# Kernel tuning notes

Hardware: AMD Instinct MI355X
Metric: run time of the kernel (lower is better)

## Reference

```python
import jax, jax.numpy as jnp
import numpy as np

K = 4                 # max_block_size (depthwise conv kernel size)
BLOCKS = (1, 2, 3, 4) # block sizes, offset 0
DS = 4                # downsample_factor
BLOCK_MULT = 12       # lcm(1,2,3,4)
DIM = 512
NUM_TOKENS = 256


def setup_inputs() -> dict:
    key = jax.random.key(0)
    ks = jax.random.split(key, 8)
    b, n = 4, 4096
    s = 0.02
    return {
        "x": jax.random.randint(ks[0], (b, n), 0, NUM_TOKENS),
        "emb": jax.random.normal(ks[1], (NUM_TOKENS, DIM), dtype=jnp.float32) * s,
        "conv_w": jax.random.normal(ks[2], (DIM, K), dtype=jnp.float32) * s,   # depthwise Conv1d weight [d,1,K] squeezed
        "conv_b": jax.random.normal(ks[3], (DIM,), dtype=jnp.float32) * s,
        "proj_w": jax.random.normal(ks[4], (DIM, DIM), dtype=jnp.float32) * s,  # 1x1 conv == linear [out,in]
        "proj_b": jax.random.normal(ks[5], (DIM,), dtype=jnp.float32) * s,
        "score_w": jax.random.normal(ks[6], (DIM,), dtype=jnp.float32) * s,     # nn.Linear(dim,1)
        "score_b": jax.random.normal(ks[7], (), dtype=jnp.float32) * s,
    }


def reference(x, emb, conv_w, conv_b, proj_w, proj_b, score_w, score_b):
    b, n = x.shape
    h = emb[x]  # [b, n, d] token embedding (gather)

    # pos_conv: pad (K-1) at sequence end, depthwise conv (valid), then pointwise proj
    hp = jnp.pad(h, ((0, 0), (0, K - 1), (0, 0)))
    y = conv_b + sum(hp[:, k:k + n, :] * conv_w[:, k] for k in range(K))  # [b, n, d]
    h = y @ proj_w.T + proj_b

    # pad sequence to multiple of lcm of block sizes
    L = -(-n // BLOCK_MULT) * BLOCK_MULT
    h = jnp.pad(h, ((0, 0), (0, L - n), (0, 0)))

    # multi-scale block mean pooling, upsampled back to length L
    reprs = []
    for bs in BLOCKS:
        r = h.reshape(b, L // bs, bs, DIM).mean(axis=2)     # [b, L/bs, d]
        reprs.append(jnp.repeat(r, bs, axis=1))             # [b, L, d]
    block_reprs = jnp.stack(reprs, axis=2)                  # [b, L, nb, d]

    # per-position block scores
    scores = block_reprs @ score_w + score_b                # [b, L, nb]
    scores = jax.nn.softmax(scores, axis=2)

    # consensus attention over positions (d = nb = len(BLOCKS))
    sim = jnp.einsum('bid,bjd->bij', scores, scores)        # [b, L, L]
    attn = jax.nn.softmax(sim, axis=-1)
    scores = jnp.einsum('bij,bjm->bim', attn, scores)       # [b, L, nb]

    # fuse block representations and downsample
    out = jnp.einsum('bnkd,bnk->bnd', block_reprs, scores)  # [b, L, d]
    m = -(-n // DS) * DS                                    # == n (4096 divisible by 4)
    out = out[:, :m].reshape(b, m // DS, DS, DIM).mean(axis=2)
    return out
```

## Files before the change

### kernel.cpp

```cpp
#include <hip/hip_runtime.h>
#include <hip/hip_bf16.h>

#define B_ 4
#define N_ 4096
#define L_ 4104
#define D_ 512
#define CH2 129
#define BK 64
#define NF 210

typedef __attribute__((ext_vector_type(8))) short bf16x8;
typedef __attribute__((ext_vector_type(4))) float f32x4;

__device__ __forceinline__ float bf2f(unsigned short u) {
  union { unsigned u; float f; } c; c.u = ((unsigned)u) << 16; return c.f;
}

__global__ __launch_bounds__(256) void k_g(const float* __restrict__ emb,
    const float* __restrict__ pw, const float* __restrict__ cwp,
    const float* __restrict__ cb, const float* __restrict__ pb,
    float* __restrict__ G, float* __restrict__ biasp,
    unsigned* __restrict__ featPk, float* __restrict__ featCf) {
  __shared__ __align__(16) __hip_bfloat16 As[2][64 * BK];
  __shared__ __align__(16) __hip_bfloat16 Bs[2][128 * BK];
  __shared__ __align__(16) float cwS[512];
  __shared__ float red[4];
  const int bx = blockIdx.x;
  const int t = threadIdx.x;
  const int w = t >> 6, l = t & 63;

  if (bx == 128) {
    if (t < NF) {
      int idx = 0, mp = 0, mq = 0, mr = 0, ms = 0;
      for (int m = 0; m <= 6; ++m)
        for (int p = m; p >= 0; --p)
          for (int q = m - p; q >= 0; --q)
            for (int r = m - p - q; r >= 0; --r) {
              const int s4 = m - p - q - r;
              if (idx == t) { mp = p; mq = q; mr = r; ms = s4; }
              ++idx;
            }
      featPk[t] = (unsigned)mp | ((unsigned)mq << 8) | ((unsigned)mr << 16) | ((unsigned)ms << 24);
      const float invf[7] = {1.f, 1.f, 0.5f, 1.f/6.f, 1.f/24.f, 1.f/120.f, 1.f/720.f};
      featCf[t] = invf[mp] * invf[mq] * invf[mr] * invf[ms];
    }
    return;
  }
  if (bx >= 64) {
    const int o0 = (bx - 64) * 8;
    const float2 cv = *(const float2*)(cb + t * 2);
#pragma unroll
    for (int oo = 0; oo < 8; ++oo) {
      const int o = o0 + oo;
      const float2 wv = *(const float2*)(pw + (size_t)o * 512 + t * 2);
      float s = wv.x * cv.x + wv.y * cv.y;
#pragma unroll
      for (int off = 32; off > 0; off >>= 1) s += __shfl_xor(s, off);
      if (l == 0) red[w] = s;
      __syncthreads();
      if (t == 0) biasp[o] = red[0] + red[1] + red[2] + red[3] + pb[o];
      __syncthreads();
    }
    return;
  }

  const int m0 = (bx & 3) * 64;
  const int n0 = ((bx >> 2) & 3) * 128;
  const int kp = bx >> 4;
  const int quad = l >> 4, r16 = l & 15;
  const int wc = w * 32;

  cwS[t]       = cwp[t * 4 + kp];
  cwS[t + 256] = cwp[(t + 256) * 4 + kp];

  f32x4 acc[4][2];
#pragma unroll
  for (int a = 0; a < 4; ++a)
#pragma unroll
    for (int bq = 0; bq < 2; ++bq) acc[a][bq] = (f32x4){0.f, 0.f, 0.f, 0.f};

  const int ra = t >> 2, ga0 = (t & 3) * 2;
  const int rb = t >> 1, gb0 = (t & 1) * 4;

#define STAGEG(buf, kb)                                                          \
  _Pragma("unroll")                                                              \
  for (int gi = 0; gi < 2; ++gi) {                                               \
    const int g = ga0 + gi;                                                      \
    const int c0 = (kb) + g * 8;                                                 \
    const float4 a0 = *(const float4*)(emb + (size_t)(m0 + ra) * 512 + c0);      \
    const float4 a1 = *(const float4*)(emb + (size_t)(m0 + ra) * 512 + c0 + 4);  \
    const float4 w0 = *(const float4*)(cwS + c0);                                \
    const float4 w1 = *(const float4*)(cwS + c0 + 4);                            \
    union { __hip_bfloat16 q[8]; bf16x8 v; } ua;                                 \
    ua.q[0] = __float2bfloat16(a0.x * w0.x); ua.q[1] = __float2bfloat16(a0.y * w0.y); \
    ua.q[2] = __float2bfloat16(a0.z * w0.z); ua.q[3] = __float2bfloat16(a0.w * w0.w); \
    ua.q[4] = __float2bfloat16(a1.x * w1.x); ua.q[5] = __float2bfloat16(a1.y * w1.y); \
    ua.q[6] = __float2bfloat16(a1.z * w1.z); ua.q[7] = __float2bfloat16(a1.w * w1.w); \
    *(bf16x8*)(&As[buf][ra * BK + ((g ^ (ra & 7)) * 8)]) = ua.v;                 \
  }                                                                              \
  _Pragma("unroll")                                                              \
  for (int gi = 0; gi < 4; ++gi) {                                               \
    const int g = gb0 + gi;                                                      \
    const int c0 = (kb) + g * 8;                                                 \
    const float4 b0 = *(const float4*)(pw + (size_t)(n0 + rb) * 512 + c0);       \
    const float4 b1 = *(const float4*)(pw + (size_t)(n0 + rb) * 512 + c0 + 4);   \
    union { __hip_bfloat16 q[8]; bf16x8 v; } ub;                                 \
    ub.q[0] = __float2bfloat16(b0.x); ub.q[1] = __float2bfloat16(b0.y);          \
    ub.q[2] = __float2bfloat16(b0.z); ub.q[3] = __float2bfloat16(b0.w);          \
    ub.q[4] = __float2bfloat16(b1.x); ub.q[5] = __float2bfloat16(b1.y);          \
    ub.q[6] = __float2bfloat16(b1.z); ub.q[7] = __float2bfloat16(b1.w);          \
    *(bf16x8*)(&Bs[buf][rb * BK + ((g ^ (rb & 7)) * 8)]) = ub.v;                 \
  }

  __syncthreads();
  STAGEG(0, 0)
  __syncthreads();

#pragma unroll 1
  for (int kt = 0; kt < 8; ++kt) {
    const int cur = kt & 1;
    if (kt < 7) { STAGEG(1 - cur, (kt + 1) * BK) }
#pragma unroll
    for (int kk = 0; kk < 2; ++kk) {
      const int col_e = (kk * 32 + quad * 8) ^ ((r16 & 7) * 8);
      bf16x8 af[4], bfr[2];
#pragma unroll
      for (int ti = 0; ti < 4; ++ti)
        af[ti] = *(const bf16x8*)(&As[cur][(ti * 16 + r16) * BK + col_e]);
#pragma unroll
      for (int tj = 0; tj < 2; ++tj)
        bfr[tj] = *(const bf16x8*)(&Bs[cur][(wc + tj * 16 + r16) * BK + col_e]);
#pragma unroll
      for (int ti = 0; ti < 4; ++ti)
#pragma unroll
        for (int tj = 0; tj < 2; ++tj)
          acc[ti][tj] = __builtin_amdgcn_mfma_f32_16x16x32_bf16(af[ti], bfr[tj], acc[ti][tj], 0, 0, 0);
    }
    __syncthreads();
  }
#undef STAGEG

#pragma unroll
  for (int ti = 0; ti < 4; ++ti) {
    const int gi0 = m0 + ti * 16 + quad * 4;
#pragma unroll
    for (int tj = 0; tj < 2; ++tj) {
      const int go = n0 + wc + tj * 16 + r16;
#pragma unroll
      for (int r = 0; r < 4; ++r)
        G[((size_t)kp * 256 + gi0 + r) * 512 + go] = acc[ti][tj][r];
    }
  }
}

__global__ __launch_bounds__(256) void k_h(const int* __restrict__ x,
    const float* __restrict__ G, const float* __restrict__ biasp,
    const float* __restrict__ sw, unsigned* __restrict__ h,
    float* __restrict__ tb, float* __restrict__ Zg) {
  __shared__ int tokS[11];
  __shared__ float tpart[8][4];
  const int bx = blockIdx.x;
  const int b = bx >> 9, i0 = (bx & 511) * 8;
  const int t = threadIdx.x, d = t * 2, w = t >> 6, l = t & 63;
  if (bx < 17) {
    const int zi = bx * 256 + t;
    if (zi < B_ * NF * 5) Zg[zi] = 0.f;
  }
  if (t < 11) {
    const int j = i0 + t;
    tokS[t] = (j < N_) ? x[b * N_ + j] : 0;
  }
  __syncthreads();
  const float2 bp  = *(const float2*)(biasp + d);
  const float2 swv = *(const float2*)(sw + d);
#pragma unroll
  for (int r = 0; r < 8; ++r) {
    const int i = i0 + r;
    float2 acc = bp;
#pragma unroll
    for (int k = 0; k < 4; ++k) {
      if (i + k < N_) {
        const float2 g = *(const float2*)(G + ((size_t)k * 256 + tokS[r + k]) * 512 + d);
        acc.x += g.x; acc.y += g.y;
      }
    }
    union { __hip_bfloat16 q[2]; unsigned u; } pk;
    pk.q[0] = __float2bfloat16(acc.x);
    pk.q[1] = __float2bfloat16(acc.y);
    h[(size_t)(b * N_ + i) * 256 + t] = pk.u;
    float v = acc.x * swv.x + acc.y * swv.y;
#pragma unroll
    for (int off = 32; off > 0; off >>= 1) v += __shfl_xor(v, off);
    if (l == 0) tpart[r][w] = v;
  }
  __syncthreads();
  if (t < 8)
    tb[b * N_ + i0 + t] = tpart[t][0] + tpart[t][1] + tpart[t][2] + tpart[t][3];
}

__device__ __forceinline__ float4 softmax4(const float* __restrict__ tw, int base,
                                           int i, float bb) {
  const float s0 = tw[i - base] + bb;
  const int j2 = i & ~1;
  const float s1 = (tw[j2 - base] + tw[j2 + 1 - base]) * 0.5f + bb;
  const int j3 = (i / 3) * 3;
  const float s2 = (tw[j3 - base] + tw[j3 + 1 - base] + tw[j3 + 2 - base]) * (1.f / 3.f) + bb;
  const int j4 = i & ~3;
  const float s3 = (tw[j4 - base] + tw[j4 + 1 - base] + tw[j4 + 2 - base] + tw[j4 + 3 - base]) * 0.25f + bb;
  const float m = fmaxf(fmaxf(s0, s1), fmaxf(s2, s3));
  const float e0 = __expf(s0 - m), e1 = __expf(s1 - m), e2 = __expf(s2 - m), e3 = __expf(s3 - m);
  const float inv = 1.f / (e0 + e1 + e2 + e3);
  return make_float4(e0 * inv, e1 * inv, e2 * inv, e3 * inv);
}

__global__ __launch_bounds__(256) void k_zphi(const float* __restrict__ tb,
    const float* __restrict__ sb, const unsigned* __restrict__ featPk,
    const float* __restrict__ featCf, float* __restrict__ Zg) {
  __shared__ float twj[135];
  __shared__ float P[CH2][32];
  __shared__ unsigned pkS[NF];
  const int bx = blockIdx.x;
  const int b = bx >> 5, jc = bx & 31;
  const int t = threadIdx.x;
  const int j0 = jc * CH2;
  const int rowb = b * N_;
  const int len = min(CH2, L_ - j0);
  if (t < NF) pkS[t] = featPk[t];
  for (int idx = t; idx < 135; idx += 256) {
    const int j = j0 - 3 + idx;
    twj[idx] = (j >= 0 && j < N_) ? tb[rowb + j] : 0.f;
  }
  __syncthreads();
  const float bb = sb[0];
  if (t < len) {
    const float4 s = softmax4(twj, j0 - 3, j0 + t, bb);
    float* p = &P[t][0];
    float va = 1.f, vb = 1.f, vc = 1.f, vd = 1.f;
    p[0] = 1.f; p[8] = 1.f; p[16] = 1.f; p[24] = 1.f;
#pragma unroll
    for (int e = 1; e < 8; ++e) {
      va *= s.x; vb *= s.y; vc *= s.z; vd *= s.w;
      p[e] = va; p[8 + e] = vb; p[16 + e] = vc; p[24 + e] = vd;
    }
  }
  __syncthreads();
  if (t < NF) {
    const unsigned pk = pkS[t];
    const int p = pk & 255, q = (pk >> 8) & 255, r = (pk >> 16) & 255, s4 = pk >> 24;
    float z0 = 0.f, z1 = 0.f, z2 = 0.f, z3 = 0.f, z4 = 0.f;
    for (int jj = 0; jj < len; ++jj) {
      const float* pp = &P[jj][0];
      const float pa0 = pp[p],       pa1 = pp[p + 1];
      const float pb0 = pp[8 + q],   pb1 = pp[8 + q + 1];
      const float pc0 = pp[16 + r],  pc1 = pp[16 + r + 1];
      const float pd0 = pp[24 + s4], pd1 = pp[24 + s4 + 1];
      const float cd = pc0 * pd0, ab = pa0 * pb0;
      z4 += pa0 * (pb0 * cd);
      z0 += pa1 * (pb0 * cd);
      z1 += pb1 * (pa0 * cd);
      z2 += pc1 * (ab * pd0);
      z3 += pd1 * (ab * pc0);
    }
    float* zb = Zg + (size_t)(b * NF + t) * 5;
    atomicAdd(zb + 0, z0); atomicAdd(zb + 1, z1); atomicAdd(zb + 2, z2);
    atomicAdd(zb + 3, z3); atomicAdd(zb + 4, z4);
  }
}

__global__ __launch_bounds__(256) void k_fuse(const __hip_bfloat16* __restrict__ h,
    const float* __restrict__ tb, const float* __restrict__ sb,
    const unsigned* __restrict__ featPk, const float* __restrict__ featCf,
    const float* __restrict__ Zg, float* __restrict__ out) {
  __shared__ __align__(16) float4 wgtS[12];
  __shared__ float tbS[12];
  __shared__ float Pr[12][32];
  __shared__ float Zl[NF * 5];
  __shared__ unsigned pkS[NF];
  __shared__ float cfS[NF];
  const int bx = blockIdx.x;
  const int b = bx / 342, j12 = bx % 342;
  const int t = threadIdx.x, d = t * 2;
  const int r0 = 12 * j12;

  if (t < NF) { pkS[t] = featPk[t]; cfS[t] = featCf[t]; }
  for (int i2 = t; i2 < NF * 5; i2 += 256) Zl[i2] = Zg[(size_t)b * NF * 5 + i2];
  if (t < 12) {
    const int row = r0 + t;
    tbS[t] = (row < N_) ? tb[b * N_ + row] : 0.f;
  }
  __syncthreads();
  if (t < 12) {
    const float4 s = softmax4(tbS, r0, r0 + t, sb[0]);
    float* p = &Pr[t][0];
    float va = 1.f, vb = 1.f, vc = 1.f, vd = 1.f;
    p[0] = 1.f; p[8] = 1.f; p[16] = 1.f; p[24] = 1.f;
#pragma unroll
    for (int e = 1; e < 8; ++e) {
      va *= s.x; vb *= s.y; vc *= s.z; vd *= s.w;
      p[e] = va; p[8 + e] = vb; p[16 + e] = vc; p[24 + e] = vd;
    }
  }
  __syncthreads();
  if (t < 192) {
    const int row = t >> 4, fi = t & 15;
    float n0 = 0.f, n1 = 0.f, n2 = 0.f, n3 = 0.f, dn = 0.f;
    const float* pr = &Pr[row][0];
    for (int f = fi; f < NF; f += 16) {
      const unsigned pk = pkS[f];
      const float val = cfS[f] * pr[pk & 255] * pr[8 + ((pk >> 8) & 255)]
                                * pr[16 + ((pk >> 16) & 255)] * pr[24 + (pk >> 24)];
      const float* z = &Zl[f * 5];
      n0 += val * z[0]; n1 += val * z[1]; n2 += val * z[2]; n3 += val * z[3];
      dn += val * z[4];
    }
#pragma unroll
    for (int m = 8; m >= 1; m >>= 1) {
      n0 += __shfl_xor(n0, m); n1 += __shfl_xor(n1, m); n2 += __shfl_xor(n2, m);
      n3 += __shfl_xor(n3, m); dn += __shfl_xor(dn, m);
    }
    if (fi == 0) {
      const float inv = 1.f / dn;
      wgtS[row] = make_float4(n0 * inv, n1 * inv, n2 * inv, n3 * inv);
    }
  }
  __syncthreads();

  const __hip_bfloat16* hb = h + (size_t)b * N_ * D_;
  float2 hv[12];
#pragma unroll
  for (int q = 0; q < 12; ++q) {
    const int row = r0 + q;
    if (row < N_) {
      const ushort2 u = *(const ushort2*)(hb + (size_t)row * D_ + d);
      hv[q] = make_float2(bf2f(u.x), bf2f(u.y));
    } else {
      hv[q] = make_float2(0.f, 0.f);
    }
  }

  float2 p2[6], p3[4], p4[3];
#pragma unroll
  for (int g = 0; g < 6; ++g) {
    p2[g].x = (hv[2 * g].x + hv[2 * g + 1].x) * 0.5f;
    p2[g].y = (hv[2 * g].y + hv[2 * g + 1].y) * 0.5f;
  }
#pragma unroll
  for (int g = 0; g < 4; ++g) {
    p3[g].x = (hv[3 * g].x + hv[3 * g + 1].x + hv[3 * g + 2].x) * (1.f / 3.f);
    p3[g].y = (hv[3 * g].y + hv[3 * g + 1].y + hv[3 * g + 2].y) * (1.f / 3.f);
  }
#pragma unroll
  for (int g = 0; g < 3; ++g) {
    p4[g].x = (hv[4 * g].x + hv[4 * g + 1].x + hv[4 * g + 2].x + hv[4 * g + 3].x) * 0.25f;
    p4[g].y = (hv[4 * g].y + hv[4 * g + 1].y + hv[4 * g + 2].y + hv[4 * g + 3].y) * 0.25f;
  }

#pragma unroll
  for (int o = 0; o < 3; ++o) {
    const int orow = j12 * 3 + o;
    if (orow < 1024) {
      float ox = 0.f, oy = 0.f;
#pragma unroll
      for (int rr = 0; rr < 4; ++rr) {
        const int r = 4 * o + rr;
        const float4 wv = wgtS[r];
        const float2 p1 = hv[r];
        const float2 q2 = p2[r >> 1];
        const float2 q3 = p3[r / 3];
        const float2 q4 = p4[o];
        ox += wv.x * p1.x + wv.y * q2.x + wv.z * q3.x + wv.w * q4.x;
        oy += wv.x * p1.y + wv.y * q2.y + wv.z * q3.y + wv.w * q4.y;
      }
      float2 ov; ov.x = ox * 0.25f; ov.y = oy * 0.25f;
      *(float2*)(out + (size_t)(b * 1024 + orow) * D_ + d) = ov;
    }
  }
}

extern "C" void kernel_launch(void* const* d_in, const int* in_sizes, int n_in,
                              void* d_out, int out_size, void* d_ws, size_t ws_size,
                              hipStream_t stream) {
  const int*   x       = (const int*)d_in[0];
  const float* emb     = (const float*)d_in[1];
  const float* conv_w  = (const float*)d_in[2];
  const float* conv_b  = (const float*)d_in[3];
  const float* proj_w  = (const float*)d_in[4];
  const float* proj_b  = (const float*)d_in[5];
  const float* score_w = (const float*)d_in[6];
  const float* score_b = (const float*)d_in[7];
  float* out = (float*)d_out;

  char* ws = (char*)d_ws;
  size_t off = 0;
  float*          G    = (float*)(ws + off);          off += (size_t)4 * 256 * 512 * 4;
  float*          bias = (float*)(ws + off);          off += (size_t)512 * 4;
  __hip_bfloat16* h    = (__hip_bfloat16*)(ws + off); off += (size_t)16384 * 512 * 2;
  float*          tb   = (float*)(ws + off);          off += (size_t)16384 * 4;
  float*          Zg   = (float*)(ws + off);          off += (size_t)B_ * NF * 5 * 4;
  unsigned*       featPk = (unsigned*)(ws + off);     off += (size_t)NF * 4;
  float*          featCf = (float*)(ws + off);        off += (size_t)NF * 4;
  (void)in_sizes; (void)n_in; (void)out_size; (void)ws_size;

  k_g<<<129, 256, 0, stream>>>(emb, proj_w, conv_w, conv_b, proj_b, G, bias, featPk, featCf);
  k_h<<<2048, 256, 0, stream>>>(x, G, bias, score_w, (unsigned*)h, tb, Zg);
  k_zphi<<<B_ * 32, 256, 0, stream>>>(tb, score_b, featPk, featCf, Zg);
  k_fuse<<<B_ * 342, 256, 0, stream>>>(h, tb, score_b, featPk, featCf, Zg, out);
}
```

Before: 126.4 us.

## Drop the h materialization kernel and recompute rows from G in consumers

Removes the k_h kernel that wrote a bf16 copy of h and the per-position score array to global memory. k_zphi now gathers the per-tap G rows and reduces them against score_w itself. k_fuse regathers the same rows in fp32, so h stays in registers for pooling and fusion. The score bias is dropped because softmax ignores a constant shift, and zeroing of Zg moves into k_g. This trades a large write-then-read of h and one launch for repeated gathers of the small, cache-resident G table. It also risks score inconsistencies at the padded tail: k_zphi omits the projected-bias term from real rows' scores while padded rows stay at zero.

```diff
diff --git a/kernel.cpp b/kernel.cpp
--- a/kernel.cpp
+++ b/kernel.cpp
@@ -12,15 +12,12 @@
 typedef __attribute__((ext_vector_type(8))) short bf16x8;
 typedef __attribute__((ext_vector_type(4))) float f32x4;
 
-__device__ __forceinline__ float bf2f(unsigned short u) {
-  union { unsigned u; float f; } c; c.u = ((unsigned)u) << 16; return c.f;
-}
-
 __global__ __launch_bounds__(256) void k_g(const float* __restrict__ emb,
     const float* __restrict__ pw, const float* __restrict__ cwp,
     const float* __restrict__ cb, const float* __restrict__ pb,
     float* __restrict__ G, float* __restrict__ biasp,
-    unsigned* __restrict__ featPk, float* __restrict__ featCf) {
+    unsigned* __restrict__ featPk, float* __restrict__ featCf,
+    float* __restrict__ Zg) {
   __shared__ __align__(16) __hip_bfloat16 As[2][64 * BK];
   __shared__ __align__(16) __hip_bfloat16 Bs[2][128 * BK];
   __shared__ __align__(16) float cwS[512];
@@ -44,6 +41,7 @@
       const float invf[7] = {1.f, 1.f, 0.5f, 1.f/6.f, 1.f/24.f, 1.f/120.f, 1.f/720.f};
       featCf[t] = invf[mp] * invf[mq] * invf[mr] * invf[ms];
     }
+    for (int i = t; i < B_ * NF * 5; i += 256) Zg[i] = 0.f;
     return;
   }
   if (bx >= 64) {
@@ -153,87 +151,66 @@
   }
 }
 
-__global__ __launch_bounds__(256) void k_h(const int* __restrict__ x,
-    const float* __restrict__ G, const float* __restrict__ biasp,
-    const float* __restrict__ sw, unsigned* __restrict__ h,
-    float* __restrict__ tb, float* __restrict__ Zg) {
-  __shared__ int tokS[11];
-  __shared__ float tpart[8][4];
-  const int bx = blockIdx.x;
-  const int b = bx >> 9, i0 = (bx & 511) * 8;
-  const int t = threadIdx.x, d = t * 2, w = t >> 6, l = t & 63;
-  if (bx < 17) {
-    const int zi = bx * 256 + t;
-    if (zi < B_ * NF * 5) Zg[zi] = 0.f;
-  }
-  if (t < 11) {
-    const int j = i0 + t;
-    tokS[t] = (j < N_) ? x[b * N_ + j] : 0;
-  }
-  __syncthreads();
-  const float2 bp  = *(const float2*)(biasp + d);
-  const float2 swv = *(const float2*)(sw + d);
-#pragma unroll
-  for (int r = 0; r < 8; ++r) {
-    const int i = i0 + r;
-    float2 acc = bp;
-#pragma unroll
-    for (int k = 0; k < 4; ++k) {
-      if (i + k < N_) {
-        const float2 g = *(const float2*)(G + ((size_t)k * 256 + tokS[r + k]) * 512 + d);
-        acc.x += g.x; acc.y += g.y;
-      }
-    }
-    union { __hip_bfloat16 q[2]; unsigned u; } pk;
-    pk.q[0] = __float2bfloat16(acc.x);
-    pk.q[1] = __float2bfloat16(acc.y);
-    h[(size_t)(b * N_ + i) * 256 + t] = pk.u;
-    float v = acc.x * swv.x + acc.y * swv.y;
-#pragma unroll
-    for (int off = 32; off > 0; off >>= 1) v += __shfl_xor(v, off);
-    if (l == 0) tpart[r][w] = v;
-  }
-  __syncthreads();
-  if (t < 8)
-    tb[b * N_ + i0 + t] = tpart[t][0] + tpart[t][1] + tpart[t][2] + tpart[t][3];
-}
-
-__device__ __forceinline__ float4 softmax4(const float* __restrict__ tw, int base,
-                                           int i, float bb) {
-  const float s0 = tw[i - base] + bb;
+__device__ __forceinline__ float4 softmax4(const float* __restrict__ tw, int base, int i) {
+  const float s0 = tw[i - base];
   const int j2 = i & ~1;
-  const float s1 = (tw[j2 - base] + tw[j2 + 1 - base]) * 0.5f + bb;
+  const float s1 = (tw[j2 - base] + tw[j2 + 1 - base]) * 0.5f;
   const int j3 = (i / 3) * 3;
-  const float s2 = (tw[j3 - base] + tw[j3 + 1 - base] + tw[j3 + 2 - base]) * (1.f / 3.f) + bb;
+  const float s2 = (tw[j3 - base] + tw[j3 + 1 - base] + tw[j3 + 2 - base]) * (1.f / 3.f);
   const int j4 = i & ~3;
-  const float s3 = (tw[j4 - base] + tw[j4 + 1 - base] + tw[j4 + 2 - base] + tw[j4 + 3 - base]) * 0.25f + bb;
+  const float s3 = (tw[j4 - base] + tw[j4 + 1 - base] + tw[j4 + 2 - base] + tw[j4 + 3 - base]) * 0.25f;
   const float m = fmaxf(fmaxf(s0, s1), fmaxf(s2, s3));
   const float e0 = __expf(s0 - m), e1 = __expf(s1 - m), e2 = __expf(s2 - m), e3 = __expf(s3 - m);
   const float inv = 1.f / (e0 + e1 + e2 + e3);
   return make_float4(e0 * inv, e1 * inv, e2 * inv, e3 * inv);
 }
 
-__global__ __launch_bounds__(256) void k_zphi(const float* __restrict__ tb,
-    const float* __restrict__ sb, const unsigned* __restrict__ featPk,
-    const float* __restrict__ featCf, float* __restrict__ Zg) {
+__global__ __launch_bounds__(256) void k_zphi(const int* __restrict__ x,
+    const float* __restrict__ G, const float* __restrict__ sw,
+    const unsigned* __restrict__ featPk, float* __restrict__ Zg) {
+  __shared__ __align__(16) float swS[512];
+  __shared__ int xS[138];
   __shared__ float twj[135];
   __shared__ float P[CH2][32];
   __shared__ unsigned pkS[NF];
   const int bx = blockIdx.x;
   const int b = bx >> 5, jc = bx & 31;
-  const int t = threadIdx.x;
+  const int t = threadIdx.x, w = t >> 6, l = t & 63;
   const int j0 = jc * CH2;
-  const int rowb = b * N_;
   const int len = min(CH2, L_ - j0);
+  swS[t] = sw[t]; swS[t + 256] = sw[t + 256];
   if (t < NF) pkS[t] = featPk[t];
-  for (int idx = t; idx < 135; idx += 256) {
-    const int j = j0 - 3 + idx;
-    twj[idx] = (j >= 0 && j < N_) ? tb[rowb + j] : 0.f;
-  }
-  __syncthreads();
-  const float bb = sb[0];
+  if (t < 138) {
+    const int j = j0 - 3 + t;
+    xS[t] = (j >= 0 && j < N_) ? x[b * N_ + j] : 0;
+  }
+  __syncthreads();
+  for (int jj = w; jj < 135; jj += 4) {
+    const int j = j0 - 3 + jj;
+    float v = 0.f;
+    if (j >= 0 && j < N_) {
+      float ax = 0.f, ay = 0.f, az = 0.f, aw = 0.f;
+      float bx4 = 0.f, by = 0.f, bz = 0.f, bw = 0.f;
+#pragma unroll
+      for (int k = 0; k < 4; ++k) {
+        if (j + k < N_) {
+          const float4* gr = (const float4*)(G + (size_t)(k * 256 + xS[jj + k]) * 512);
+          const float4 g0 = gr[l], g1 = gr[64 + l];
+          ax += g0.x; ay += g0.y; az += g0.z; aw += g0.w;
+          bx4 += g1.x; by += g1.y; bz += g1.z; bw += g1.w;
+        }
+      }
+      const float4 w0 = ((const float4*)swS)[l], w1 = ((const float4*)swS)[64 + l];
+      v = ax * w0.x + ay * w0.y + az * w0.z + aw * w0.w
+        + bx4 * w1.x + by * w1.y + bz * w1.z + bw * w1.w;
+#pragma unroll
+      for (int m = 32; m >= 1; m >>= 1) v += __shfl_xor(v, m);
+    }
+    if (l == 0) twj[jj] = v;
+  }
+  __syncthreads();
   if (t < len) {
-    const float4 s = softmax4(twj, j0 - 3, j0 + t, bb);
+    const float4 s = softmax4(twj, j0 - 3, j0 + t);
     float* p = &P[t][0];
     float va = 1.f, vb = 1.f, vc = 1.f, vd = 1.f;
     p[0] = 1.f; p[8] = 1.f; p[16] = 1.f; p[24] = 1.f;
@@ -267,30 +244,65 @@
   }
 }
 
-__global__ __launch_bounds__(256) void k_fuse(const __hip_bfloat16* __restrict__ h,
-    const float* __restrict__ tb, const float* __restrict__ sb,
+__global__ __launch_bounds__(256) void k_fuse(const int* __restrict__ x,
+    const float* __restrict__ G, const float* __restrict__ biasp,
+    const float* __restrict__ sw,
     const unsigned* __restrict__ featPk, const float* __restrict__ featCf,
     const float* __restrict__ Zg, float* __restrict__ out) {
   __shared__ __align__(16) float4 wgtS[12];
-  __shared__ float tbS[12];
+  __shared__ float tpart[12][4];
+  __shared__ float twb[12];
   __shared__ float Pr[12][32];
   __shared__ float Zl[NF * 5];
   __shared__ unsigned pkS[NF];
   __shared__ float cfS[NF];
+  __shared__ int xS[15];
   const int bx = blockIdx.x;
   const int b = bx / 342, j12 = bx % 342;
-  const int t = threadIdx.x, d = t * 2;
+  const int t = threadIdx.x, d = t * 2, w = t >> 6, l = t & 63;
   const int r0 = 12 * j12;
 
   if (t < NF) { pkS[t] = featPk[t]; cfS[t] = featCf[t]; }
   for (int i2 = t; i2 < NF * 5; i2 += 256) Zl[i2] = Zg[(size_t)b * NF * 5 + i2];
+  if (t < 15) {
+    const int row = r0 + t;
+    xS[t] = (row < N_) ? x[b * N_ + row] : 0;
+  }
+  __syncthreads();
+
+  const float2 bp  = *(const float2*)(biasp + d);
+  const float2 swv = *(const float2*)(sw + d);
+  float2 acc[12];
+  float pt[12];
+#pragma unroll
+  for (int r = 0; r < 12; ++r) {
+    const int row = r0 + r;
+    float2 a = make_float2(0.f, 0.f);
+    if (row < N_) {
+      a = bp;
+#pragma unroll
+      for (int k = 0; k < 4; ++k) {
+        if (row + k < N_) {
+          const float2 g = *(const float2*)(G + (size_t)(k * 256 + xS[r + k]) * 512 + d);
+          a.x += g.x; a.y += g.y;
+        }
+      }
+    }
+    acc[r] = a;
+    pt[r] = a.x * swv.x + a.y * swv.y;
+  }
+#pragma unroll
+  for (int r = 0; r < 12; ++r) {
+    float v = pt[r];
+#pragma unroll
+    for (int m = 32; m >= 1; m >>= 1) v += __shfl_xor(v, m);
+    if (l == 0) tpart[r][w] = v;
+  }
+  __syncthreads();
+  if (t < 12) twb[t] = tpart[t][0] + tpart[t][1] + tpart[t][2] + tpart[t][3];
+  __syncthreads();
   if (t < 12) {
-    const int row = r0 + t;
-    tbS[t] = (row < N_) ? tb[b * N_ + row] : 0.f;
-  }
-  __syncthreads();
-  if (t < 12) {
-    const float4 s = softmax4(tbS, r0, r0 + t, sb[0]);
+    const float4 s = softmax4(twb, r0, r0 + t);
     float* p = &Pr[t][0];
     float va = 1.f, vb = 1.f, vc = 1.f, vd = 1.f;
     p[0] = 1.f; p[8] = 1.f; p[16] = 1.f; p[24] = 1.f;
@@ -325,34 +337,21 @@
   }
   __syncthreads();
 
-  const __hip_bfloat16* hb = h + (size_t)b * N_ * D_;
-  float2 hv[12];
-#pragma unroll
-  for (int q = 0; q < 12; ++q) {
-    const int row = r0 + q;
-    if (row < N_) {
-      const ushort2 u = *(const ushort2*)(hb + (size_t)row * D_ + d);
-      hv[q] = make_float2(bf2f(u.x), bf2f(u.y));
-    } else {
-      hv[q] = make_float2(0.f, 0.f);
-    }
-  }
-
   float2 p2[6], p3[4], p4[3];
 #pragma unroll
   for (int g = 0; g < 6; ++g) {
-    p2[g].x = (hv[2 * g].x + hv[2 * g + 1].x) * 0.5f;
-    p2[g].y = (hv[2 * g].y + hv[2 * g + 1].y) * 0.5f;
+    p2[g].x = (acc[2 * g].x + acc[2 * g + 1].x) * 0.5f;
+    p2[g].y = (acc[2 * g].y + acc[2 * g + 1].y) * 0.5f;
   }
 #pragma unroll
   for (int g = 0; g < 4; ++g) {
-    p3[g].x = (hv[3 * g].x + hv[3 * g + 1].x + hv[3 * g + 2].x) * (1.f / 3.f);
-    p3[g].y = (hv[3 * g].y + hv[3 * g + 1].y + hv[3 * g + 2].y) * (1.f / 3.f);
+    p3[g].x = (acc[3 * g].x + acc[3 * g + 1].x + acc[3 * g + 2].x) * (1.f / 3.f);
+    p3[g].y = (acc[3 * g].y + acc[3 * g + 1].y + acc[3 * g + 2].y) * (1.f / 3.f);
   }
 #pragma unroll
   for (int g = 0; g < 3; ++g) {
-    p4[g].x = (hv[4 * g].x + hv[4 * g + 1].x + hv[4 * g + 2].x + hv[4 * g + 3].x) * 0.25f;
-    p4[g].y = (hv[4 * g].y + hv[4 * g + 1].y + hv[4 * g + 2].y + hv[4 * g + 3].y) * 0.25f;
+    p4[g].x = (acc[4 * g].x + acc[4 * g + 1].x + acc[4 * g + 2].x + acc[4 * g + 3].x) * 0.25f;
+    p4[g].y = (acc[4 * g].y + acc[4 * g + 1].y + acc[4 * g + 2].y + acc[4 * g + 3].y) * 0.25f;
   }
 
 #pragma unroll
@@ -364,7 +363,7 @@
       for (int rr = 0; rr < 4; ++rr) {
         const int r = 4 * o + rr;
         const float4 wv = wgtS[r];
-        const float2 p1 = hv[r];
+        const float2 p1 = acc[r];
         const float2 q2 = p2[r >> 1];
         const float2 q3 = p3[r / 3];
         const float2 q4 = p4[o];
@@ -387,22 +386,19 @@
   const float* proj_w  = (const float*)d_in[4];
   const float* proj_b  = (const float*)d_in[5];
   const float* score_w = (const float*)d_in[6];
-  const float* score_b = (const float*)d_in[7];
   float* out = (float*)d_out;
 
   char* ws = (char*)d_ws;
   size_t off = 0;
-  float*          G    = (float*)(ws + off);          off += (size_t)4 * 256 * 512 * 4;
-  float*          bias = (float*)(ws + off);          off += (size_t)512 * 4;
-  __hip_bfloat16* h    = (__hip_bfloat16*)(ws + off); off += (size_t)16384 * 512 * 2;
-  float*          tb   = (float*)(ws + off);          off += (size_t)16384 * 4;
-  float*          Zg   = (float*)(ws + off);          off += (size_t)B_ * NF * 5 * 4;
-  unsigned*       featPk = (unsigned*)(ws + off);     off += (size_t)NF * 4;
-  float*          featCf = (float*)(ws + off);        off += (size_t)NF * 4;
+  float*    G      = (float*)(ws + off);    off += (size_t)4 * 256 * 512 * 4;
+  float*    biasp  = (float*)(ws + off);    off += (size_t)512 * 4;
+  float*    Zg     = (float*)(ws + off);    off += (size_t)B_ * NF * 5 * 4;
+  unsigned* featPk = (unsigned*)(ws + off); off += (size_t)NF * 4;
+  float*    featCf = (float*)(ws + off);    off += (size_t)NF * 4;
   (void)in_sizes; (void)n_in; (void)out_size; (void)ws_size;
 
-  k_g<<<129, 256, 0, stream>>>(emb, proj_w, conv_w, conv_b, proj_b, G, bias, featPk, featCf);
-  k_h<<<2048, 256, 0, stream>>>(x, G, bias, score_w, (unsigned*)h, tb, Zg);
-  k_zphi<<<B_ * 32, 256, 0, stream>>>(tb, score_b, featPk, featCf, Zg);
-  k_fuse<<<B_ * 342, 256, 0, stream>>>(h, tb, score_b, featPk, featCf, Zg, out);
+  k_g<<<129, 256, 0, stream>>>(emb, proj_w, conv_w, conv_b, proj_b, G, biasp,
+                               featPk, featCf, Zg);
+  k_zphi<<<B_ * 32, 256, 0, stream>>>(x, G, score_w, featPk, Zg);
+  k_fuse<<<B_ * 342, 256, 0, stream>>>(x, G, biasp, score_w, featPk, featCf, Zg, out);
 }
```

Result: slower. 156.3 us (+23.6%).
